# Kernel tuning notes

Hardware: AMD Instinct MI355X
Metric: run time of the kernel (lower is better)

The kernel has to match this reference:

```python
import jax, jax.numpy as jnp
import numpy as np

WS = 8        # window_size
SHIFT = 4     # shift_size
NH = 6        # num_heads
EPS = 1e-5


def _rel_pos_index(ws):
    coords = np.stack(np.meshgrid(np.arange(ws), np.arange(ws), indexing='ij'))  # [2,ws,ws]
    cf = coords.reshape(2, -1)                      # [2, ws*ws]
    rel = cf[:, :, None] - cf[:, None, :]           # [2, N, N]
    rel = rel.transpose(1, 2, 0)                    # [N, N, 2]
    rel[:, :, 0] += ws - 1
    rel[:, :, 1] += ws - 1
    rel[:, :, 0] *= 2 * ws - 1
    return rel.sum(-1)                              # [N, N] int


def _attn_mask(H, W, ws, shift):
    img = np.zeros((H, W), dtype=np.float32)
    slices = (slice(0, -ws), slice(-ws, -shift), slice(-shift, None))
    cnt = 0
    for hs in slices:
        for wsl in slices:
            img[hs, wsl] = cnt
            cnt += 1
    mw = img.reshape(H // ws, ws, W // ws, ws).transpose(0, 2, 1, 3).reshape(-1, ws * ws)
    diff = mw[:, None, :] - mw[:, :, None]          # [nW, N, N]
    return np.where(diff != 0, -100.0, 0.0).astype(np.float32)


def _layernorm(x, g, b):
    mu = x.mean(-1, keepdims=True)
    var = ((x - mu) ** 2).mean(-1, keepdims=True)
    return (x - mu) * jax.lax.rsqrt(var + EPS) * g + b


def setup_inputs() -> dict:
    key = jax.random.key(0)
    ks = jax.random.split(key, 8)
    C, HID = 192, 768
    return {
        'x': jax.random.normal(ks[0], (8, 128, 128, C), jnp.float32),
        'g1': jnp.ones((C,), jnp.float32),
        'b1': jnp.zeros((C,), jnp.float32),
        'qkv_w': jax.random.normal(ks[1], (3 * C, C), jnp.float32) * 0.02,
        'qkv_b': jnp.zeros((3 * C,), jnp.float32),
        'rpb_table': jax.random.normal(ks[2], ((2 * WS - 1) ** 2, NH), jnp.float32) * 0.02,
        'proj_w': jax.random.normal(ks[3], (C, C), jnp.float32) * 0.02,
        'proj_b': jnp.zeros((C,), jnp.float32),
        'g2': jnp.ones((C,), jnp.float32),
        'b2': jnp.zeros((C,), jnp.float32),
        'fc1_w': jax.random.normal(ks[4], (HID, C), jnp.float32) * 0.02,
        'fc1_b': jnp.zeros((HID,), jnp.float32),
        'fc2_w': jax.random.normal(ks[5], (C, HID), jnp.float32) * 0.02,
        'fc2_b': jnp.zeros((C,), jnp.float32),
    }


def reference(x, g1, b1, qkv_w, qkv_b, rpb_table, proj_w, proj_b, g2, b2,
              fc1_w, fc1_b, fc2_w, fc2_b):
    B, H, W, C = x.shape
    N = WS * WS
    hd = C // NH
    scale = hd ** -0.5

    rpi = jnp.asarray(_rel_pos_index(WS))                 # [N,N] static
    mask = jnp.asarray(_attn_mask(H, W, WS, SHIFT))       # [nW,N,N] static
    nW = mask.shape[0]

    shortcut = x.reshape(B, H * W, C)
    xn = _layernorm(shortcut, g1, b1).reshape(B, H, W, C)

    # cyclic shift
    xs = jnp.roll(xn, shift=(-SHIFT, -SHIFT), axis=(1, 2))

    # window partition -> [B*nW, N, C]
    win = xs.reshape(B, H // WS, WS, W // WS, WS, C).transpose(0, 1, 3, 2, 4, 5)
    win = win.reshape(-1, N, C)
    B_ = win.shape[0]

    # qkv
    qkv = jnp.einsum('bnc,oc->bno', win, qkv_w) + qkv_b   # [B_,N,3C]
    qkv = qkv.reshape(B_, N, 3, NH, hd).transpose(2, 0, 3, 1, 4)  # [3,B_,NH,N,hd]
    q, k, v = qkv[0] * scale, qkv[1], qkv[2]

    attn = jnp.einsum('bhnd,bhmd->bhnm', q, k)            # [B_,NH,N,N]
    bias = rpb_table[rpi.reshape(-1)].reshape(N, N, NH).transpose(2, 0, 1)
    attn = attn + bias[None]
    attn = attn.reshape(B, nW, NH, N, N) + mask[None, :, None]
    attn = jax.nn.softmax(attn.reshape(B_, NH, N, N), axis=-1)

    out = jnp.einsum('bhnm,bhmd->bhnd', attn, v)          # [B_,NH,N,hd]
    out = out.transpose(0, 2, 1, 3).reshape(B_, N, C)
    out = jnp.einsum('bnc,oc->bno', out, proj_w) + proj_b

    # window reverse -> [B,H,W,C]
    out = out.reshape(B, H // WS, W // WS, WS, WS, C).transpose(0, 1, 3, 2, 4, 5)
    out = out.reshape(B, H, W, C)
    out = jnp.roll(out, shift=(SHIFT, SHIFT), axis=(1, 2)).reshape(B, H * W, C)

    x1 = shortcut + out
    h = _layernorm(x1, g2, b2)
    h = jnp.einsum('bnc,hc->bnh', h, fc1_w) + fc1_b
    h = jax.nn.gelu(h, approximate=False)
    h = jnp.einsum('bnh,ch->bnc', h, fc2_w) + fc2_b
    x2 = x1 + h
    return x2.reshape(B, H, W, C)
```

## Files before the change

### kernel.cpp

```cpp
#include <hip/hip_runtime.h>
#include <hip/hip_bf16.h>

typedef __attribute__((ext_vector_type(8))) short s16x8;
typedef __attribute__((ext_vector_type(4))) float f32x4;

__device__ __forceinline__ unsigned short f2bf(float f){
    __hip_bfloat16 h = __float2bfloat16(f);
    return *reinterpret_cast<unsigned short*>(&h);
}

__device__ __forceinline__ int flab(int g){ return (g < 120) ? 0 : ((g < 124) ? 1 : 2); }

__device__ __forceinline__ void async16(const void* g, void* l){
    __builtin_amdgcn_global_load_lds(
        (const __attribute__((address_space(1))) unsigned int*)g,
        (__attribute__((address_space(3))) unsigned int*)l, 16, 0, 0);
}

__global__ __launch_bounds__(256) void wconv_all(
    const float* __restrict__ w0, const float* __restrict__ w1,
    const float* __restrict__ w2, const float* __restrict__ w3,
    unsigned short* __restrict__ o0, unsigned short* __restrict__ o1,
    unsigned short* __restrict__ o2, unsigned short* __restrict__ o3)
{
    int i = blockIdx.x*256 + threadIdx.x;
    if (i < 110592) o0[i] = f2bf(w0[i]);
    if (i < 36864)  o1[i] = f2bf(w1[i]);
    if (i < 147456) o2[i] = f2bf(w2[i]);
    if (i < 147456) o3[i] = f2bf(w3[i]);
}

__global__ __launch_bounds__(256) void lnqkv_kernel(
    const float* __restrict__ x, const float* __restrict__ g1, const float* __restrict__ b1,
    const unsigned short* __restrict__ wq, const float* __restrict__ qkvb,
    unsigned short* __restrict__ qo, unsigned short* __restrict__ ko,
    unsigned short* __restrict__ vo)
{
    __shared__ __attribute__((aligned(16))) unsigned short win[64*200];
    __shared__ __attribute__((aligned(16))) unsigned short Bs[64*200];
    const int b_ = blockIdx.x;
    const int bb = b_>>8, wi = b_&255, wh = wi>>4, ww = wi&15;
    const int tid = threadIdx.x;
    const int wv = tid>>6, lane = tid&63, lrow = lane&15, quad = lane>>4;

    {
        const int n = tid>>2, q4 = tid&3;
        const int r = n>>3, c = n&7;
        const int hh = (wh*8 + r + 4)&127, wp = (ww*8 + c + 4)&127;
        const float* px = x + (((size_t)bb*128+hh)*128+wp)*192 + q4*48;
        float v[48];
        #pragma unroll
        for (int m=0;m<12;++m) *(float4*)(v+m*4) = *(const float4*)(px+m*4);
        float s = 0.f;
        #pragma unroll
        for (int k=0;k<48;++k) s += v[k];
        s += __shfl_xor(s,1); s += __shfl_xor(s,2);
        float mu = s*(1.0f/192.0f);
        float qv = 0.f;
        #pragma unroll
        for (int k=0;k<48;++k){ float d=v[k]-mu; qv += d*d; }
        qv += __shfl_xor(qv,1); qv += __shfl_xor(qv,2);
        float rstd = rsqrtf(qv*(1.0f/192.0f) + 1e-5f);
        const float* pg = g1 + q4*48;
        const float* pb = b1 + q4*48;
        unsigned short* pw = win + n*200 + q4*48;
        #pragma unroll
        for (int k=0;k<48;++k) pw[k] = f2bf((v[k]-mu)*rstd*pg[k] + pb[k]);
    }
    __syncthreads();

    s16x8 af[6];
    #pragma unroll
    for (int kc=0;kc<6;++kc)
        af[kc] = *(const s16x8*)(win + (wv*16+lrow)*200 + kc*32 + quad*8);

    for (int ot=0; ot<9; ++ot) {
        const int o0 = ot*64;
        __syncthreads();
        #pragma unroll
        for (int t=0;t<6;++t) {
            int cid = tid + t*256;
            *(int4*)(Bs + (cid/24)*200 + (cid%24)*8) =
                *(const int4*)(wq + (size_t)o0*192 + cid*8);
        }
        __syncthreads();
        f32x4 acc[4];
        #pragma unroll
        for (int j=0;j<4;++j) acc[j] = (f32x4){0.f,0.f,0.f,0.f};
        #pragma unroll
        for (int kc=0;kc<6;++kc)
            #pragma unroll
            for (int j=0;j<4;++j) {
                s16x8 bf = *(const s16x8*)(Bs + (j*16+lrow)*200 + kc*32 + quad*8);
                acc[j] = __builtin_amdgcn_mfma_f32_16x16x32_bf16(af[kc], bf, acc[j], 0, 0, 0);
            }
        __syncthreads();
        unsigned short* T = Bs;
        const int part = ot/3;
        float bv[4];
        #pragma unroll
        for (int j=0;j<4;++j) bv[j] = qkvb[o0 + j*16 + lrow];

        if (part < 2) {
            const float scale = (part==0) ? 0.17677669529663687f : 1.0f;
            #pragma unroll
            for (int j=0;j<4;++j)
                #pragma unroll
                for (int rg=0;rg<4;++rg) {
                    int n2 = wv*16 + quad*4 + rg;
                    T[n2*72 + j*16 + lrow] = f2bf((acc[j][rg]+bv[j])*scale);
                }
            __syncthreads();
            unsigned short* dst = (part==0) ? qo : ko;
            #pragma unroll
            for (int t=0;t<2;++t) {
                int c = tid + t*256;
                int n2 = c>>3, blk = c&7;
                int o_in = o0 + blk*8 - part*192;
                int head = o_in>>5, d = o_in&31;
                *(int4*)(dst + (((size_t)b_*6+head)*64 + n2)*32 + d) =
                    *(const int4*)(T + n2*72 + blk*8);
            }
        } else {
            #pragma unroll
            for (int j=0;j<4;++j)
                #pragma unroll
                for (int rg=0;rg<4;++rg) {
                    int n2 = wv*16 + quad*4 + rg;
                    T[(j*16+lrow)*72 + n2] = f2bf(acc[j][rg]+bv[j]);
                }
            __syncthreads();
            #pragma unroll
            for (int t=0;t<2;++t) {
                int c = tid + t*256;
                int ol = c>>3, nb = (c&7)*8;
                int o_in = o0 + ol - 384;
                int head = o_in>>5, d = o_in&31;
                *(int4*)(vo + (((size_t)b_*6+head)*32 + d)*64 + nb) =
                    *(const int4*)(T + ol*72 + nb);
            }
        }
    }
}

__global__ __launch_bounds__(384) void attn_kernel(
    const unsigned short* __restrict__ q, const unsigned short* __restrict__ k,
    const unsigned short* __restrict__ vT, const float* __restrict__ rpb,
    unsigned short* __restrict__ ao)
{
    __shared__ float rpb_s[1350];
    __shared__ __attribute__((aligned(16))) unsigned short p_lds[6*4608];
    const int b_ = blockIdx.x;
    const int h = threadIdx.x >> 6;
    const int lane = threadIdx.x & 63, lrow = lane & 15, quad = lane >> 4;
    for (int i = threadIdx.x; i < 1350; i += 384) rpb_s[i] = rpb[i];
    __syncthreads();

    const size_t hb = ((size_t)b_*6 + h)*2048;
    const unsigned short* qb = q  + hb;
    const unsigned short* kb = k  + hb;
    const unsigned short* vb = vT + hb;

    s16x8 qf[4], kf[4];
    #pragma unroll
    for (int i = 0; i < 4; ++i) qf[i] = *(const s16x8*)(qb + (i*16+lrow)*32 + quad*8);
    #pragma unroll
    for (int j = 0; j < 4; ++j) kf[j] = *(const s16x8*)(kb + (j*16+lrow)*32 + quad*8);

    const f32x4 zz = {0.f,0.f,0.f,0.f};
    f32x4 s[4][4];
    #pragma unroll
    for (int i = 0; i < 4; ++i)
        #pragma unroll
        for (int j = 0; j < 4; ++j)
            s[i][j] = __builtin_amdgcn_mfma_f32_16x16x32_bf16(qf[i], kf[j], zz, 0, 0, 0);

    const int wi = b_ & 255, wh = wi >> 4, ww = wi & 15;
    int labm[4];
    #pragma unroll
    for (int j = 0; j < 4; ++j) {
        int m = j*16 + lrow;
        labm[j] = flab(wh*8 + (m >> 3))*3 + flab(ww*8 + (m & 7));
    }
    unsigned short* pl = p_lds + h*4608;
    #pragma unroll
    for (int i = 0; i < 4; ++i) {
        #pragma unroll
        for (int rg = 0; rg < 4; ++rg) {
            int n = i*16 + quad*4 + rg;
            int rn = n >> 3, cn = n & 7;
            int labn = flab(wh*8 + rn)*3 + flab(ww*8 + cn);
            float vals[4];
            float vmax = -1e30f;
            #pragma unroll
            for (int j = 0; j < 4; ++j) {
                int m = j*16 + lrow;
                int idx = ((rn - (m >> 3) + 7)*15 + (cn - (m & 7) + 7))*6 + h;
                float val = s[i][j][rg] + rpb_s[idx];
                if (labn != labm[j]) val -= 100.f;
                vals[j] = val;
                vmax = fmaxf(vmax, val);
            }
            #pragma unroll
            for (int o = 1; o < 16; o <<= 1) vmax = fmaxf(vmax, __shfl_xor(vmax, o));
            float sum = 0.f;
            #pragma unroll
            for (int j = 0; j < 4; ++j) { vals[j] = __expf(vals[j] - vmax); sum += vals[j]; }
            #pragma unroll
            for (int o = 1; o < 16; o <<= 1) sum += __shfl_xor(sum, o);
            float inv = 1.f / sum;
            #pragma unroll
            for (int j = 0; j < 4; ++j) pl[n*72 + j*16 + lrow] = f2bf(vals[j]*inv);
        }
    }
    __syncthreads();

    f32x4 oacc[4][2];
    #pragma unroll
    for (int i = 0; i < 4; ++i) { oacc[i][0] = zz; oacc[i][1] = zz; }
    #pragma unroll
    for (int kc = 0; kc < 2; ++kc) {
        s16x8 vf[2];
        #pragma unroll
        for (int jd = 0; jd < 2; ++jd)
            vf[jd] = *(const s16x8*)(vb + (jd*16+lrow)*64 + kc*32 + quad*8);
        #pragma unroll
        for (int i = 0; i < 4; ++i) {
            s16x8 pf = *(const s16x8*)(pl + (i*16+lrow)*72 + kc*32 + quad*8);
            #pragma unroll
            for (int jd = 0; jd < 2; ++jd)
                oacc[i][jd] = __builtin_amdgcn_mfma_f32_16x16x32_bf16(pf, vf[jd], oacc[i][jd], 0, 0, 0);
        }
    }
    unsigned short* ob = ao + (size_t)b_*12288 + h*32;
    #pragma unroll
    for (int i = 0; i < 4; ++i)
        #pragma unroll
        for (int jd = 0; jd < 2; ++jd)
            #pragma unroll
            for (int rg = 0; rg < 4; ++rg) {
                int n = i*16 + quad*4 + rg;
                ob[(size_t)n*192 + jd*16 + lrow] = f2bf(oacc[i][jd][rg]);
            }
}

__device__ __forceinline__ void mm64x192(
    const unsigned short* __restrict__ A, const unsigned short* __restrict__ W,
    size_t m0, unsigned short* As, unsigned short* Bs, f32x4 (&acc)[12])
{
    const int tid = threadIdx.x, wv = tid>>6, lane = tid&63;
    const int lrow = lane&15, quad = lane>>4;
    const int grow = lane>>2;
    const int gcb  = (lane&3) ^ ((lane>>3)&3);
    #pragma unroll
    for (int j=0;j<12;++j) acc[j] = (f32x4){0.f,0.f,0.f,0.f};

    const unsigned short* Ab = A + (m0 + grow)*192 + gcb*8;
    const unsigned short* Wb = W + (size_t)grow*192 + gcb*8;

    auto issue = [&](int k0, unsigned short* Ad, unsigned short* Bd) {
        async16(Ab + (size_t)(wv*16)*192 + k0,     Ad + wv*512);
        async16(Wb + (size_t)(wv*16)*192 + k0,     Bd + wv*512);
        async16(Wb + (size_t)((wv+4)*16)*192 + k0, Bd + (wv+4)*512);
        async16(Wb + (size_t)((wv+8)*16)*192 + k0, Bd + (wv+8)*512);
    };
    issue(0, As, Bs);
    int cur = 0;
    for (int k0=0; k0<192; k0+=32) {
        __syncthreads();
        if (k0+32 < 192) issue(k0+32, As + (cur^1)*2048, Bs + (cur^1)*6144);
        const unsigned short* Ac = As + cur*2048;
        const unsigned short* Bc = Bs + cur*6144;
        const int rs = (quad ^ ((lrow>>1)&3)) << 3;
        s16x8 af = *(const s16x8*)(Ac + (wv*16+lrow)*32 + rs);
        #pragma unroll
        for (int j=0;j<12;++j) {
            s16x8 bf = *(const s16x8*)(Bc + (j*16+lrow)*32 + rs);
            acc[j] = __builtin_amdgcn_mfma_f32_16x16x32_bf16(af, bf, acc[j], 0, 0, 0);
        }
        cur ^= 1;
    }
}

__global__ __launch_bounds__(256) void projln_kernel(
    const unsigned short* __restrict__ A, const unsigned short* __restrict__ W,
    const float* __restrict__ pbias, const float* __restrict__ x,
    const float* __restrict__ g2, const float* __restrict__ b2,
    float* __restrict__ x1, unsigned short* __restrict__ xln2)
{
    __shared__ __attribute__((aligned(16))) char smem[32768];
    unsigned short* As = (unsigned short*)smem;
    unsigned short* Bs = (unsigned short*)(smem + 8192);
    const int b_ = blockIdx.x;
    const int tid = threadIdx.x, wv = tid>>6, lane = tid&63;
    const int lrow = lane&15, quad = lane>>4;
    const size_t m0 = (size_t)b_*64;

    f32x4 acc[12];
    mm64x192(A, W, m0, As, Bs, acc);
    __syncthreads();

    const int bb = b_>>8, wi = b_&255, wh = wi>>4, ww = wi&15;
    float bv[12], gv[12], b2v[12];
    #pragma unroll
    for (int j=0;j<12;++j) {
        bv[j]  = pbias[j*16+lrow];
        gv[j]  = g2[j*16+lrow];
        b2v[j] = b2[j*16+lrow];
    }
    unsigned short* T = (unsigned short*)smem;
    #pragma unroll
    for (int rg=0;rg<4;++rg) {
        int n2 = wv*16 + quad*4 + rg;
        int r = n2>>3, c = n2&7;
        int hh = (wh*8+r+4)&127, wp = (ww*8+c+4)&127;
        size_t tok = ((size_t)bb*128+hh)*128 + wp;
        float xv[12];
        float s = 0.f;
        #pragma unroll
        for (int j=0;j<12;++j) {
            float t = acc[j][rg] + bv[j] + x[tok*192 + j*16 + lrow];
            xv[j] = t; s += t;
        }
        #pragma unroll
        for (int o=1;o<16;o<<=1) s += __shfl_xor(s, o);
        float mu = s*(1.0f/192.0f);
        float qv = 0.f;
        #pragma unroll
        for (int j=0;j<12;++j){ float d = xv[j]-mu; qv += d*d; }
        #pragma unroll
        for (int o=1;o<16;o<<=1) qv += __shfl_xor(qv, o);
        float rstd = rsqrtf(qv*(1.0f/192.0f) + 1e-5f);
        #pragma unroll
        for (int j=0;j<12;++j) {
            x1[tok*192 + j*16 + lrow] = xv[j];
            T[n2*200 + j*16 + lrow] = f2bf((xv[j]-mu)*rstd*gv[j] + b2v[j]);
        }
    }
    __syncthreads();
    #pragma unroll
    for (int t=0;t<6;++t) {
        int cid = tid + t*256;
        int n2 = cid/24, blk = cid%24;
        int r = n2>>3, c = n2&7;
        int hh = (wh*8+r+4)&127, wp = (ww*8+c+4)&127;
        size_t tok = ((size_t)bb*128+hh)*128 + wp;
        *(int4*)(xln2 + tok*192 + blk*8) = *(const int4*)(T + n2*200 + blk*8);
    }
}

template<int K>
__device__ __forceinline__ void mm128x96(
    const unsigned short* __restrict__ A, const unsigned short* __restrict__ W,
    size_t m0, int o0, unsigned short* As, unsigned short* Bs,
    f32x4 (&acc)[2][6])
{
    const int tid = threadIdx.x, wv = tid>>6, lane = tid&63;
    const int lrow = lane&15, quad = lane>>4;
    const int grow = lane>>2;
    const int gcb  = (lane&3) ^ ((lane>>3)&3);
    #pragma unroll
    for (int i=0;i<2;++i)
        #pragma unroll
        for (int j=0;j<6;++j) acc[i][j] = (f32x4){0.f,0.f,0.f,0.f};

    const unsigned short* Ab = A + (m0 + grow)*(size_t)K + gcb*8;
    const unsigned short* Wb = W + ((size_t)(o0 + grow))*K + gcb*8;

    auto issue = [&](int k0, unsigned short* Ad, unsigned short* Bd) {
        async16(Ab + (size_t)(wv*16)*K + k0,     Ad + wv*512);
        async16(Ab + (size_t)((wv+4)*16)*K + k0, Ad + (wv+4)*512);
        async16(Wb + (size_t)(wv*16)*K + k0,     Bd + wv*512);
        if (wv < 2)
            async16(Wb + (size_t)((wv+4)*16)*K + k0, Bd + (wv+4)*512);
    };
    issue(0, As, Bs);
    int cur = 0;
    for (int k0=0; k0<K; k0+=32) {
        __syncthreads();
        if (k0+32 < K) issue(k0+32, As + (cur^1)*4096, Bs + (cur^1)*3072);
        const unsigned short* Ac = As + cur*4096;
        const unsigned short* Bc = Bs + cur*3072;
        const int rs = (quad ^ ((lrow>>1)&3)) << 3;
        s16x8 af[2], bf[6];
        #pragma unroll
        for (int i=0;i<2;++i)
            af[i] = *(const s16x8*)(Ac + (wv*32 + i*16 + lrow)*32 + rs);
        #pragma unroll
        for (int j=0;j<6;++j)
            bf[j] = *(const s16x8*)(Bc + (j*16 + lrow)*32 + rs);
        #pragma unroll
        for (int i=0;i<2;++i)
            #pragma unroll
            for (int j=0;j<6;++j)
                acc[i][j] = __builtin_amdgcn_mfma_f32_16x16x32_bf16(af[i], bf[j], acc[i][j], 0, 0, 0);
        cur ^= 1;
    }
}

__global__ __launch_bounds__(256, 4) void gemm_fc1_kernel(
    const unsigned short* __restrict__ A, const unsigned short* __restrict__ Wm,
    const float* __restrict__ bias, unsigned short* __restrict__ h1)
{
    __shared__ __attribute__((aligned(16))) char smem[28672];
    unsigned short* As = (unsigned short*)smem;
    unsigned short* Bs = (unsigned short*)(smem + 16384);
    const int bid = blockIdx.x;
    const int virt = (bid & 7)*1024 + (bid >> 3);
    const size_t m0 = (size_t)(virt >> 3)*128;
    const int o0 = (virt & 7)*96;
    f32x4 acc[2][6];
    mm128x96<192>(A, Wm, m0, o0, As, Bs, acc);
    const int tid = threadIdx.x, wv = tid>>6, lane = tid&63;
    const int lrow = lane&15, quad = lane>>4;
    float bv[6];
    #pragma unroll
    for (int j=0;j<6;++j) bv[j] = bias[o0 + j*16 + lrow];
    __syncthreads();
    unsigned short* T = (unsigned short*)smem;
    #pragma unroll
    for (int i=0;i<2;++i)
        #pragma unroll
        for (int j=0;j<6;++j)
            #pragma unroll
            for (int rg=0;rg<4;++rg) {
                int ml = wv*32 + i*16 + quad*4 + rg;
                float v = acc[i][j][rg] + bv[j];
                float v2 = v*v;
                float z = v*(1.5957691216057308f + 0.07135481627f*v2);
                float r = v * __builtin_amdgcn_rcpf(1.f + __expf(-z));
                T[ml*104 + j*16 + lrow] = f2bf(r);
            }
    __syncthreads();
    #pragma unroll
    for (int t=0;t<6;++t) {
        int c = tid + t*256;
        int row = c/12, blk = c%12;
        *(int4*)(h1 + (m0+row)*768 + o0 + blk*8) = *(const int4*)(T + row*104 + blk*8);
    }
}

__global__ __launch_bounds__(256, 4) void gemm_fc2_kernel(
    const unsigned short* __restrict__ A, const unsigned short* __restrict__ Wm,
    const float* __restrict__ bias, const float* __restrict__ x1, float* __restrict__ out)
{
    __shared__ __attribute__((aligned(16))) char smem[28672];
    unsigned short* As = (unsigned short*)smem;
    unsigned short* Bs = (unsigned short*)(smem + 16384);
    const int bid = blockIdx.x;
    const int virt = (bid & 7)*256 + (bid >> 3);
    const size_t m0 = (size_t)(virt >> 1)*128;
    const int o0 = (virt & 1)*96;
    f32x4 acc[2][6];
    mm128x96<768>(A, Wm, m0, o0, As, Bs, acc);
    const int tid = threadIdx.x, wv = tid>>6, lane = tid&63;
    const int lrow = lane&15, quad = lane>>4;
    float bv[6];
    #pragma unroll
    for (int j=0;j<6;++j) bv[j] = bias[o0 + j*16 + lrow];
    float* T = (float*)smem;
    #pragma unroll
    for (int p=0;p<2;++p) {
        __syncthreads();
        if ((wv>>1) == p) {
            int wl = wv&1;
            #pragma unroll
            for (int i=0;i<2;++i)
                #pragma unroll
                for (int j=0;j<6;++j)
                    #pragma unroll
                    for (int rg=0;rg<4;++rg)
                        T[(wl*32 + i*16 + quad*4 + rg)*100 + j*16 + lrow] = acc[i][j][rg] + bv[j];
        }
        __syncthreads();
        #pragma unroll
        for (int t=0;t<6;++t) {
            int c = tid + t*256;
            int row = c/24, blk = c%24;
            size_t ad = (m0 + p*64 + row)*192 + o0 + blk*4;
            float4 v = *(const float4*)(T + row*100 + blk*4);
            float4 rx = *(const float4*)(x1 + ad);
            v.x += rx.x; v.y += rx.y; v.z += rx.z; v.w += rx.w;
            *(float4*)(out + ad) = v;
        }
    }
}

extern "C" void kernel_launch(void* const* d_in, const int* in_sizes, int n_in,
                              void* d_out, int out_size, void* d_ws, size_t ws_size,
                              hipStream_t stream)
{
    const float* x      = (const float*)d_in[0];
    const float* g1     = (const float*)d_in[1];
    const float* b1     = (const float*)d_in[2];
    const float* qkv_w  = (const float*)d_in[3];
    const float* qkv_b  = (const float*)d_in[4];
    const float* rpb    = (const float*)d_in[5];
    const float* proj_w = (const float*)d_in[6];
    const float* proj_b = (const float*)d_in[7];
    const float* g2     = (const float*)d_in[8];
    const float* b2     = (const float*)d_in[9];
    const float* fc1_w  = (const float*)d_in[10];
    const float* fc1_b  = (const float*)d_in[11];
    const float* fc2_w  = (const float*)d_in[12];
    const float* fc2_b  = (const float*)d_in[13];
    float* out = (float*)d_out;
    char* ws = (char*)d_ws;

    if (ws_size < 353206272ULL) return;

    unsigned short* qbuf  = (unsigned short*)(ws + 0);
    unsigned short* kbuf  = (unsigned short*)(ws + 50331648);
    unsigned short* vbuf  = (unsigned short*)(ws + 100663296);
    unsigned short* attnO = (unsigned short*)(ws + 150994944);
    float*          x1    = (float*)        (ws + 201326592);
    unsigned short* xln2  = (unsigned short*)(ws + 301989888);
    unsigned short* wq    = (unsigned short*)(ws + 352321536);
    unsigned short* wp    = (unsigned short*)(ws + 352321536 + 221184);
    unsigned short* w1    = (unsigned short*)(ws + 352321536 + 221184 + 73728);
    unsigned short* w2    = (unsigned short*)(ws + 352321536 + 221184 + 73728 + 294912);
    unsigned short* h1    = (unsigned short*)(ws + 0);

    wconv_all<<<576, 256, 0, stream>>>(qkv_w, proj_w, fc1_w, fc2_w, wq, wp, w1, w2);
    lnqkv_kernel<<<2048, 256, 0, stream>>>(x, g1, b1, wq, qkv_b, qbuf, kbuf, vbuf);
    attn_kernel<<<2048, 384, 0, stream>>>(qbuf, kbuf, vbuf, rpb, attnO);
    projln_kernel<<<2048, 256, 0, stream>>>(attnO, wp, proj_b, x, g2, b2, x1, xln2);
    gemm_fc1_kernel<<<8192, 256, 0, stream>>>(xln2, w1, fc1_b, h1);
    gemm_fc2_kernel<<<2048, 256, 0, stream>>>(h1, w2, fc2_b, x1, out);
}
```

Baseline: 564.3 us.

## Store xln2 and h1 in pre-swizzled tile-blocked layout; widen fc2 tile to full N

projln and fc1 now write their bf16 outputs as contiguous, pre-swizzled 128x32 k-slabs that match the LDS tile image, so the next GEMM can async-load each 64-lane wave chunk as one contiguous run. The fc2 GEMM now covers all 192 output columns per 128-row tile, so h1 rows are read once instead of twice. Its epilogue writes results directly from registers, with no LDS staging. The cost is larger LDS and register use in fc2 (occupancy drops to 3 blocks), and the direct scalar stores to out and loads from x1 are less coalesced.

Measured after the change: 575.6 us. 1.02x slower.

```diff
diff --git a/kernel.cpp b/kernel.cpp
--- a/kernel.cpp
+++ b/kernel.cpp
@@ -286,7 +286,7 @@
     const unsigned short* __restrict__ A, const unsigned short* __restrict__ W,
     const float* __restrict__ pbias, const float* __restrict__ x,
     const float* __restrict__ g2, const float* __restrict__ b2,
-    float* __restrict__ x1, unsigned short* __restrict__ xln2)
+    float* __restrict__ x1, unsigned short* __restrict__ xln2b)
 {
     __shared__ __attribute__((aligned(16))) char smem[32768];
     unsigned short* As = (unsigned short*)smem;
@@ -345,74 +345,68 @@
         int r = n2>>3, c = n2&7;
         int hh = (wh*8+r+4)&127, wp = (ww*8+c+4)&127;
         size_t tok = ((size_t)bb*128+hh)*128 + wp;
-        *(int4*)(xln2 + tok*192 + blk*8) = *(const int4*)(T + n2*200 + blk*8);
-    }
-}
-
-template<int K>
-__device__ __forceinline__ void mm128x96(
-    const unsigned short* __restrict__ A, const unsigned short* __restrict__ W,
-    size_t m0, int o0, unsigned short* As, unsigned short* Bs,
-    f32x4 (&acc)[2][6])
-{
-    const int tid = threadIdx.x, wv = tid>>6, lane = tid&63;
-    const int lrow = lane&15, quad = lane>>4;
-    const int grow = lane>>2;
-    const int gcb  = (lane&3) ^ ((lane>>3)&3);
-    #pragma unroll
-    for (int i=0;i<2;++i)
-        #pragma unroll
-        for (int j=0;j<6;++j) acc[i][j] = (f32x4){0.f,0.f,0.f,0.f};
-
-    const unsigned short* Ab = A + (m0 + grow)*(size_t)K + gcb*8;
-    const unsigned short* Wb = W + ((size_t)(o0 + grow))*K + gcb*8;
-
-    auto issue = [&](int k0, unsigned short* Ad, unsigned short* Bd) {
-        async16(Ab + (size_t)(wv*16)*K + k0,     Ad + wv*512);
-        async16(Ab + (size_t)((wv+4)*16)*K + k0, Ad + (wv+4)*512);
-        async16(Wb + (size_t)(wv*16)*K + k0,     Bd + wv*512);
-        if (wv < 2)
-            async16(Wb + (size_t)((wv+4)*16)*K + k0, Bd + (wv+4)*512);
-    };
-    issue(0, As, Bs);
-    int cur = 0;
-    for (int k0=0; k0<K; k0+=32) {
-        __syncthreads();
-        if (k0+32 < K) issue(k0+32, As + (cur^1)*4096, Bs + (cur^1)*3072);
-        const unsigned short* Ac = As + cur*4096;
-        const unsigned short* Bc = Bs + cur*3072;
-        const int rs = (quad ^ ((lrow>>1)&3)) << 3;
-        s16x8 af[2], bf[6];
-        #pragma unroll
-        for (int i=0;i<2;++i)
-            af[i] = *(const s16x8*)(Ac + (wv*32 + i*16 + lrow)*32 + rs);
-        #pragma unroll
-        for (int j=0;j<6;++j)
-            bf[j] = *(const s16x8*)(Bc + (j*16 + lrow)*32 + rs);
-        #pragma unroll
-        for (int i=0;i<2;++i)
-            #pragma unroll
-            for (int j=0;j<6;++j)
-                acc[i][j] = __builtin_amdgcn_mfma_f32_16x16x32_bf16(af[i], bf[j], acc[i][j], 0, 0, 0);
-        cur ^= 1;
+        int row = (int)(tok & 127);
+        int ks = blk>>2, kb = blk&3;
+        int sw = (kb ^ ((row>>1)&3)) << 3;
+        *(int4*)(xln2b + (tok>>7)*24576 + ks*4096 + row*32 + sw) =
+            *(const int4*)(T + n2*200 + blk*8);
     }
 }
 
 __global__ __launch_bounds__(256, 4) void gemm_fc1_kernel(
-    const unsigned short* __restrict__ A, const unsigned short* __restrict__ Wm,
-    const float* __restrict__ bias, unsigned short* __restrict__ h1)
+    const unsigned short* __restrict__ Ablk, const unsigned short* __restrict__ Wm,
+    const float* __restrict__ bias, unsigned short* __restrict__ h1b)
 {
     __shared__ __attribute__((aligned(16))) char smem[28672];
     unsigned short* As = (unsigned short*)smem;
     unsigned short* Bs = (unsigned short*)(smem + 16384);
     const int bid = blockIdx.x;
     const int virt = (bid & 7)*1024 + (bid >> 3);
-    const size_t m0 = (size_t)(virt >> 3)*128;
+    const int mt = virt >> 3;
     const int o0 = (virt & 7)*96;
-    f32x4 acc[2][6];
-    mm128x96<192>(A, Wm, m0, o0, As, Bs, acc);
     const int tid = threadIdx.x, wv = tid>>6, lane = tid&63;
     const int lrow = lane&15, quad = lane>>4;
+    const int grow = lane>>2, gcb = (lane&3)^((lane>>3)&3);
+
+    const unsigned short* Asrc = Ablk + (size_t)mt*24576 + lane*8;
+    const unsigned short* Wb = Wm + (size_t)(o0 + grow)*192 + gcb*8;
+
+    f32x4 acc[2][6];
+    #pragma unroll
+    for (int i=0;i<2;++i)
+        #pragma unroll
+        for (int j=0;j<6;++j) acc[i][j] = (f32x4){0.f,0.f,0.f,0.f};
+
+    auto issue = [&](int ks, unsigned short* Ad, unsigned short* Bd) {
+        async16(Asrc + ks*4096 + wv*512,     Ad + wv*512);
+        async16(Asrc + ks*4096 + (wv+4)*512, Ad + (wv+4)*512);
+        async16(Wb + (size_t)(wv*16)*192 + ks*32, Bd + wv*512);
+        if (wv < 2)
+            async16(Wb + (size_t)((wv+4)*16)*192 + ks*32, Bd + (wv+4)*512);
+    };
+    issue(0, As, Bs);
+    int cur = 0;
+    for (int ks=0; ks<6; ++ks) {
+        __syncthreads();
+        if (ks < 5) issue(ks+1, As + (cur^1)*4096, Bs + (cur^1)*3072);
+        const unsigned short* Ac = As + cur*4096;
+        const unsigned short* Bc = Bs + cur*3072;
+        const int rs = (quad ^ ((lrow>>1)&3)) << 3;
+        s16x8 af[2], bf[6];
+        #pragma unroll
+        for (int i=0;i<2;++i)
+            af[i] = *(const s16x8*)(Ac + (wv*32 + i*16 + lrow)*32 + rs);
+        #pragma unroll
+        for (int j=0;j<6;++j)
+            bf[j] = *(const s16x8*)(Bc + (j*16 + lrow)*32 + rs);
+        #pragma unroll
+        for (int i=0;i<2;++i)
+            #pragma unroll
+            for (int j=0;j<6;++j)
+                acc[i][j] = __builtin_amdgcn_mfma_f32_16x16x32_bf16(af[i], bf[j], acc[i][j], 0, 0, 0);
+        cur ^= 1;
+    }
+
     float bv[6];
     #pragma unroll
     for (int j=0;j<6;++j) bv[j] = bias[o0 + j*16 + lrow];
@@ -432,58 +426,84 @@
                 T[ml*104 + j*16 + lrow] = f2bf(r);
             }
     __syncthreads();
+    unsigned short* hb = h1b + (size_t)mt*98304 + (o0>>5)*4096;
     #pragma unroll
     for (int t=0;t<6;++t) {
         int c = tid + t*256;
         int row = c/12, blk = c%12;
-        *(int4*)(h1 + (m0+row)*768 + o0 + blk*8) = *(const int4*)(T + row*104 + blk*8);
-    }
-}
-
-__global__ __launch_bounds__(256, 4) void gemm_fc2_kernel(
-    const unsigned short* __restrict__ A, const unsigned short* __restrict__ Wm,
+        int ks = blk>>2, kb = blk&3;
+        int sw = (kb ^ ((row>>1)&3)) << 3;
+        *(int4*)(hb + ks*4096 + row*32 + sw) = *(const int4*)(T + row*104 + blk*8);
+    }
+}
+
+__global__ __launch_bounds__(256, 3) void gemm_fc2_kernel(
+    const unsigned short* __restrict__ Ablk, const unsigned short* __restrict__ Wm,
     const float* __restrict__ bias, const float* __restrict__ x1, float* __restrict__ out)
 {
-    __shared__ __attribute__((aligned(16))) char smem[28672];
+    __shared__ __attribute__((aligned(16))) char smem[40960];
     unsigned short* As = (unsigned short*)smem;
     unsigned short* Bs = (unsigned short*)(smem + 16384);
     const int bid = blockIdx.x;
-    const int virt = (bid & 7)*256 + (bid >> 3);
-    const size_t m0 = (size_t)(virt >> 1)*128;
-    const int o0 = (virt & 1)*96;
-    f32x4 acc[2][6];
-    mm128x96<768>(A, Wm, m0, o0, As, Bs, acc);
+    const int virt = (bid & 7)*128 + (bid >> 3);
+    const size_t m0 = (size_t)virt*128;
     const int tid = threadIdx.x, wv = tid>>6, lane = tid&63;
     const int lrow = lane&15, quad = lane>>4;
-    float bv[6];
-    #pragma unroll
-    for (int j=0;j<6;++j) bv[j] = bias[o0 + j*16 + lrow];
-    float* T = (float*)smem;
-    #pragma unroll
-    for (int p=0;p<2;++p) {
+    const int grow = lane>>2, gcb = (lane&3)^((lane>>3)&3);
+
+    const unsigned short* Asrc = Ablk + (size_t)virt*98304 + lane*8;
+    const unsigned short* Wb = Wm + (size_t)grow*768 + gcb*8;
+
+    f32x4 acc[2][12];
+    #pragma unroll
+    for (int i=0;i<2;++i)
+        #pragma unroll
+        for (int j=0;j<12;++j) acc[i][j] = (f32x4){0.f,0.f,0.f,0.f};
+
+    auto issue = [&](int ks, unsigned short* Ad, unsigned short* Bd) {
+        async16(Asrc + ks*4096 + wv*512,     Ad + wv*512);
+        async16(Asrc + ks*4096 + (wv+4)*512, Ad + (wv+4)*512);
+        #pragma unroll
+        for (int it=0;it<3;++it) {
+            int seg = wv + it*4;
+            async16(Wb + (size_t)(seg*16)*768 + ks*32, Bd + seg*512);
+        }
+    };
+    issue(0, As, Bs);
+    int cur = 0;
+    for (int ks=0; ks<24; ++ks) {
         __syncthreads();
-        if ((wv>>1) == p) {
-            int wl = wv&1;
-            #pragma unroll
-            for (int i=0;i<2;++i)
-                #pragma unroll
-                for (int j=0;j<6;++j)
-                    #pragma unroll
-                    for (int rg=0;rg<4;++rg)
-                        T[(wl*32 + i*16 + quad*4 + rg)*100 + j*16 + lrow] = acc[i][j][rg] + bv[j];
-        }
-        __syncthreads();
-        #pragma unroll
-        for (int t=0;t<6;++t) {
-            int c = tid + t*256;
-            int row = c/24, blk = c%24;
-            size_t ad = (m0 + p*64 + row)*192 + o0 + blk*4;
-            float4 v = *(const float4*)(T + row*100 + blk*4);
-            float4 rx = *(const float4*)(x1 + ad);
-            v.x += rx.x; v.y += rx.y; v.z += rx.z; v.w += rx.w;
-            *(float4*)(out + ad) = v;
-        }
-    }
+        if (ks < 23) issue(ks+1, As + (cur^1)*4096, Bs + (cur^1)*6144);
+        const unsigned short* Ac = As + cur*4096;
+        const unsigned short* Bc = Bs + cur*6144;
+        const int rs = (quad ^ ((lrow>>1)&3)) << 3;
+        s16x8 af[2], bf[12];
+        #pragma unroll
+        for (int i=0;i<2;++i)
+            af[i] = *(const s16x8*)(Ac + (wv*32 + i*16 + lrow)*32 + rs);
+        #pragma unroll
+        for (int j=0;j<12;++j)
+            bf[j] = *(const s16x8*)(Bc + (j*16 + lrow)*32 + rs);
+        #pragma unroll
+        for (int i=0;i<2;++i)
+            #pragma unroll
+            for (int j=0;j<12;++j)
+                acc[i][j] = __builtin_amdgcn_mfma_f32_16x16x32_bf16(af[i], bf[j], acc[i][j], 0, 0, 0);
+        cur ^= 1;
+    }
+
+    float bv[12];
+    #pragma unroll
+    for (int j=0;j<12;++j) bv[j] = bias[j*16 + lrow];
+    #pragma unroll
+    for (int i=0;i<2;++i)
+        #pragma unroll
+        for (int j=0;j<12;++j)
+            #pragma unroll
+            for (int rg=0;rg<4;++rg) {
+                size_t ad = (m0 + wv*32 + i*16 + quad*4 + rg)*192 + j*16 + lrow;
+                out[ad] = acc[i][j][rg] + bv[j] + x1[ad];
+            }
 }
 
 extern "C" void kernel_launch(void* const* d_in, const int* in_sizes, int n_in,
@@ -526,5 +546,5 @@
     attn_kernel<<<2048, 384, 0, stream>>>(qbuf, kbuf, vbuf, rpb, attnO);
     projln_kernel<<<2048, 256, 0, stream>>>(attnO, wp, proj_b, x, g2, b2, x1, xln2);
     gemm_fc1_kernel<<<8192, 256, 0, stream>>>(xln2, w1, fc1_b, h1);
-    gemm_fc2_kernel<<<2048, 256, 0, stream>>>(h1, w2, fc2_b, x1, out);
-}
+    gemm_fc2_kernel<<<1024, 256, 0, stream>>>(h1, w2, fc2_b, x1, out);
+}
```
